# Performance work log

Measured on AMD Instinct MI355X. Metric: run time of the kernel, lower is better.

## Reference

```python
import jax, jax.numpy as jnp
import numpy as np

N_NODES = 50000
N_EDGES = 800000
D_IN = 128
D_OUT = 128


def setup_inputs() -> dict:
    key = jax.random.key(0)
    k1, k2, k3, k4, k5, k6 = jax.random.split(key, 6)
    curr_fea = jax.random.normal(k1, (N_NODES, D_IN), dtype=jnp.float32)
    edge_index = jax.random.randint(k2, (2, N_EDGES), 0, N_NODES, dtype=jnp.int64)
    s = 1.0 / np.sqrt(D_IN)
    W_self = jax.random.uniform(k3, (D_OUT, D_IN), jnp.float32, -s, s)
    b_self = jax.random.uniform(k4, (D_OUT,), jnp.float32, -s, s)
    W_neig = jax.random.uniform(k5, (D_OUT, D_IN), jnp.float32, -s, s)
    b_neig = jax.random.uniform(k6, (D_OUT,), jnp.float32, -s, s)
    return {"curr_fea": curr_fea, "edge_index": edge_index,
            "W_self": W_self, "b_self": b_self,
            "W_neig": W_neig, "b_neig": b_neig}


def reference(curr_fea, edge_index, W_self, b_self, W_neig, b_neig):
    num_nodes = curr_fea.shape[0]
    src, dst = edge_index[0], edge_index[1]
    # symmetrize: messages flow both directions
    src_all = jnp.concatenate([src, dst], axis=0)  # [2E]
    dst_all = jnp.concatenate([dst, src], axis=0)  # [2E]
    # gather neighbor features then scatter-add into destination nodes
    nei_sum = jax.ops.segment_sum(curr_fea[src_all], dst_all,
                                  num_segments=num_nodes)  # [N, d]
    out = (curr_fea @ W_self.T + b_self) + (nei_sum @ W_neig.T + b_neig)
    return out
```

## Files before the change

### kernel.cpp

```cpp
#include <hip/hip_runtime.h>

#define DD 128
#define BM 64
#define BK 32
#define BKN 64
#define NBMAX 1024
#define ECH 4096
#define CAP 2304

typedef __attribute__((ext_vector_type(8))) short bf16x8;
typedef __attribute__((ext_vector_type(4))) float f32x4;

__device__ __forceinline__ unsigned short f2b(float x) {
    unsigned u = __float_as_uint(x);
    u += 0x7fffu + ((u >> 16) & 1u);
    return (unsigned short)(u >> 16);
}
__device__ __forceinline__ float b2f_lo(unsigned v) { return __uint_as_float(v << 16); }
__device__ __forceinline__ float b2f_hi(unsigned v) { return __uint_as_float(v & 0xffff0000u); }

__global__ void detect_kernel(const unsigned long long* __restrict__ ei,
                              int n64, int* __restrict__ flag) {
    int i = threadIdx.x;
    bool big = (i < n64) && (ei[i] >= (1ULL << 32));
    unsigned long long b = __ballot(big);
    if (i == 0) *flag = (b == 0ULL) ? 1 : 0;
}

__global__ void cvt_fea_kernel(const float* __restrict__ in,
                               unsigned short* __restrict__ out, int n4) {
    int i = blockIdx.x * 256 + threadIdx.x;
    if (i >= n4) return;
    float4 v = reinterpret_cast<const float4*>(in)[i];
    ushort4 o;
    o.x = f2b(v.x); o.y = f2b(v.y); o.z = f2b(v.z); o.w = f2b(v.w);
    reinterpret_cast<ushort4*>(out)[i] = o;
}

__global__ void cvt_w_kernel(const float* __restrict__ Ws,
                             const float* __restrict__ Wn,
                             unsigned short* __restrict__ Wcat) {
    int i = blockIdx.x * 256 + threadIdx.x;
    int n = i >> 8, k = i & 255;
    float v = (k < DD) ? Ws[n * DD + k] : Wn[n * DD + (k - DD)];
    Wcat[i] = f2b(v);
}

__launch_bounds__(256)
__global__ void bin_kernel(const void* __restrict__ ei_raw, int E,
                           const int* __restrict__ flag,
                           unsigned* __restrict__ region,
                           unsigned* __restrict__ gcur, int nbk) {
    __shared__ unsigned stage[2 * ECH];
    __shared__ unsigned cnt[NBMAX];
    __shared__ unsigned start[NBMAX];
    __shared__ unsigned cursor[NBMAX];
    __shared__ unsigned gbase[NBMAX];
    __shared__ unsigned scanT[256];

    const int t = threadIdx.x;
    for (int b = t; b < NBMAX; b += 256) { cnt[b] = 0; cursor[b] = 0; gbase[b] = 0; }
    __syncthreads();

    const int e0 = blockIdx.x * ECH;
    const int rf = *flag;
    int es[16], ed[16];
#pragma unroll
    for (int j = 0; j < 16; ++j) {
        int e = e0 + j * 256 + t;
        if (e < E) {
            if (rf) {
                const long long* p = (const long long*)ei_raw;
                es[j] = (int)p[e]; ed[j] = (int)p[e + E];
            } else {
                const int* p = (const int*)ei_raw;
                es[j] = p[e]; ed[j] = p[e + E];
            }
            atomicAdd(&cnt[ed[j] >> 6], 1u);
            atomicAdd(&cnt[es[j] >> 6], 1u);
        } else {
            es[j] = -1; ed[j] = -1;
        }
    }
    __syncthreads();

    unsigned lv[4]; unsigned lsum = 0;
#pragma unroll
    for (int j = 0; j < 4; ++j) { lv[j] = cnt[t * 4 + j]; lsum += lv[j]; }
    scanT[t] = lsum; __syncthreads();
    for (int o = 1; o < 256; o <<= 1) {
        unsigned x = (t >= o) ? scanT[t - o] : 0;
        __syncthreads();
        scanT[t] += x;
        __syncthreads();
    }
    unsigned run = scanT[t] - lsum;
#pragma unroll
    for (int j = 0; j < 4; ++j) { start[t * 4 + j] = run; run += lv[j]; }
    __syncthreads();

#pragma unroll
    for (int j = 0; j < 16; ++j) {
        if (es[j] >= 0) {
            int s = es[j], d = ed[j];
            unsigned p0 = atomicAdd(&cursor[d >> 6], 1u);
            stage[start[d >> 6] + p0] = (unsigned)(d & 63) | ((unsigned)s << 6);
            unsigned p1 = atomicAdd(&cursor[s >> 6], 1u);
            stage[start[s >> 6] + p1] = (unsigned)(s & 63) | ((unsigned)d << 6);
        }
    }
    __syncthreads();

    for (int b = t; b < nbk; b += 256) {
        unsigned c = cnt[b];
        if (c) gbase[b] = atomicAdd(&gcur[b], c);
    }
    __syncthreads();

    const int w = t >> 6, lane = t & 63;
    for (int b = w; b < nbk; b += 4) {
        unsigned c = cnt[b];
        if (!c) continue;
        unsigned gb = gbase[b], st = start[b];
        for (unsigned l2 = lane; l2 < c; l2 += 64) {
            unsigned idx = gb + l2;
            if (idx < CAP)
                region[(size_t)b * CAP + idx] = stage[st + l2];
        }
    }
}

__launch_bounds__(256)
__global__ void nodesort_kernel(unsigned* __restrict__ region,
                                const unsigned* __restrict__ gcur,
                                unsigned* __restrict__ off32, int M) {
    __shared__ unsigned ent[CAP];
    __shared__ unsigned srt[CAP];
    __shared__ unsigned c64[BKN];
    __shared__ unsigned p64[BKN + 1];
    __shared__ unsigned cur64[BKN];

    const int t = threadIdx.x, b = blockIdx.x;
    unsigned cnt = gcur[b];
    if (cnt > CAP) cnt = CAP;
    unsigned* reg = region + (size_t)b * CAP;

    for (unsigned i = t; i < cnt; i += 256) ent[i] = reg[i];
    if (t < BKN) { c64[t] = 0; cur64[t] = 0; }
    __syncthreads();

    for (unsigned i = t; i < cnt; i += 256) atomicAdd(&c64[ent[i] & 63u], 1u);
    __syncthreads();

    if (t == 0) {
        unsigned r = 0;
        for (int n = 0; n < BKN; ++n) { p64[n] = r; r += c64[n]; }
        p64[BKN] = r;
    }
    __syncthreads();

    if (t < BKN) {
        int g = b * BKN + t;
        if (g < M) off32[g] = p64[t] | (c64[t] << 12);
    }

    for (unsigned i = t; i < cnt; i += 256) {
        unsigned e = ent[i];
        unsigned p = atomicAdd(&cur64[e & 63u], 1u);
        srt[p64[e & 63u] + p] = e >> 6;
    }
    __syncthreads();

    for (unsigned i = t; i < cnt; i += 256) reg[i] = srt[i];
}

__launch_bounds__(256)
__global__ void gather_r_kernel(const unsigned short* __restrict__ feaB,
                                const unsigned* __restrict__ region,
                                const unsigned* __restrict__ off32,
                                unsigned short* __restrict__ neiB, int N) {
    int w = (int)((blockIdx.x * 256 + threadIdx.x) >> 6);
    if (w >= N) return;
    int lane = threadIdx.x & 63;
    unsigned v = off32[w];
    const unsigned* lp = region + (size_t)(w >> 6) * CAP + (v & 4095u);
    unsigned cnt = v >> 12;
    float ax = 0.f, ay = 0.f;
    const unsigned short* base = feaB + lane * 2;
    unsigned j = 0;
    for (; j + 8 <= cnt; j += 8) {
        unsigned s0 = lp[j], s1 = lp[j+1], s2 = lp[j+2], s3 = lp[j+3];
        unsigned s4 = lp[j+4], s5 = lp[j+5], s6 = lp[j+6], s7 = lp[j+7];
        unsigned a0 = *reinterpret_cast<const unsigned*>(base + (size_t)s0 * DD);
        unsigned a1 = *reinterpret_cast<const unsigned*>(base + (size_t)s1 * DD);
        unsigned a2 = *reinterpret_cast<const unsigned*>(base + (size_t)s2 * DD);
        unsigned a3 = *reinterpret_cast<const unsigned*>(base + (size_t)s3 * DD);
        unsigned a4 = *reinterpret_cast<const unsigned*>(base + (size_t)s4 * DD);
        unsigned a5 = *reinterpret_cast<const unsigned*>(base + (size_t)s5 * DD);
        unsigned a6 = *reinterpret_cast<const unsigned*>(base + (size_t)s6 * DD);
        unsigned a7 = *reinterpret_cast<const unsigned*>(base + (size_t)s7 * DD);
        ax += b2f_lo(a0) + b2f_lo(a1) + b2f_lo(a2) + b2f_lo(a3)
            + b2f_lo(a4) + b2f_lo(a5) + b2f_lo(a6) + b2f_lo(a7);
        ay += b2f_hi(a0) + b2f_hi(a1) + b2f_hi(a2) + b2f_hi(a3)
            + b2f_hi(a4) + b2f_hi(a5) + b2f_hi(a6) + b2f_hi(a7);
    }
    for (; j < cnt; ++j) {
        unsigned a = *reinterpret_cast<const unsigned*>(base + (size_t)lp[j] * DD);
        ax += b2f_lo(a); ay += b2f_hi(a);
    }
    ushort2 o; o.x = f2b(ax); o.y = f2b(ay);
    *reinterpret_cast<ushort2*>(neiB + (size_t)w * DD + lane * 2) = o;
}

__global__ void transpose_kernel(const float* __restrict__ Ws,
                                 const float* __restrict__ Wn,
                                 float* __restrict__ Wts,
                                 float* __restrict__ Wtn) {
    int idx = blockIdx.x * blockDim.x + threadIdx.x;
    int i = idx & (DD * DD - 1);
    int col = i >> 7;
    int k = i & (DD - 1);
    if (idx < DD * DD)          Wts[k * DD + col] = Ws[i];
    else if (idx < 2 * DD * DD) Wtn[k * DD + col] = Wn[i];
}

__global__ void hist_kernel(const void* __restrict__ ei_raw,
                            int* __restrict__ deg, int E,
                            const int* __restrict__ flag) {
    int e = blockIdx.x * 256 + threadIdx.x;
    if (e >= E) return;
    int s, d;
    if (*flag) {
        const long long* ei = (const long long*)ei_raw;
        s = (int)ei[e]; d = (int)ei[e + E];
    } else {
        const int* ei = (const int*)ei_raw;
        s = ei[e]; d = ei[e + E];
    }
    atomicAdd(&deg[s], 1);
    atomicAdd(&deg[d], 1);
}

__global__ void scan1_kernel(const int* __restrict__ deg, int* __restrict__ off,
                             int* __restrict__ bsum, int N) {
    __shared__ int sd[256];
    int base = blockIdx.x * 1024;
    int t = threadIdx.x;
    int v[4]; int s = 0;
#pragma unroll
    for (int j = 0; j < 4; ++j) {
        int idx = base + t * 4 + j;
        v[j] = (idx < N) ? deg[idx] : 0;
        s += v[j];
    }
    sd[t] = s; __syncthreads();
    for (int o = 1; o < 256; o <<= 1) {
        int x = (t >= o) ? sd[t - o] : 0;
        __syncthreads();
        sd[t] += x;
        __syncthreads();
    }
    int run = sd[t] - s;
    if (t == 255) bsum[blockIdx.x] = sd[255];
#pragma unroll
    for (int j = 0; j < 4; ++j) {
        int idx = base + t * 4 + j;
        if (idx < N) off[idx] = run;
        run += v[j];
    }
}

__global__ void scan2_kernel(int* __restrict__ bsum, int NB,
                             int* __restrict__ total) {
    __shared__ int sd[256];
    int t = threadIdx.x;
    int v = (t < NB) ? bsum[t] : 0;
    sd[t] = v; __syncthreads();
    for (int o = 1; o < 256; o <<= 1) {
        int x = (t >= o) ? sd[t - o] : 0;
        __syncthreads();
        sd[t] += x;
        __syncthreads();
    }
    if (t < NB) bsum[t] = sd[t] - v;
    if (t == 255) *total = sd[255];
}

__global__ void scan3_kernel(int* __restrict__ off, const int* __restrict__ bsum,
                             int N) {
    int i = blockIdx.x * blockDim.x + threadIdx.x;
    if (i < N) off[i] += bsum[i >> 10];
}

__global__ void fill_kernel(const void* __restrict__ ei_raw,
                            const int* __restrict__ off,
                            int* __restrict__ cursor, int* __restrict__ list,
                            int E, const int* __restrict__ flag) {
    int e = blockIdx.x * 256 + threadIdx.x;
    if (e >= E) return;
    int s, d;
    if (*flag) {
        const long long* ei = (const long long*)ei_raw;
        s = (int)ei[e]; d = (int)ei[e + E];
    } else {
        const int* ei = (const int*)ei_raw;
        s = ei[e]; d = ei[e + E];
    }
    int p0 = atomicAdd(&cursor[d], 1); list[off[d] + p0] = s;
    int p1 = atomicAdd(&cursor[s], 1); list[off[s] + p1] = d;
}

__launch_bounds__(256)
__global__ void gather_b_kernel(const unsigned short* __restrict__ feaB,
                                const int* __restrict__ off,
                                const int* __restrict__ list,
                                unsigned short* __restrict__ neiB, int N) {
    int w = (int)((blockIdx.x * 256 + threadIdx.x) >> 6);
    if (w >= N) return;
    int lane = threadIdx.x & 63;
    int start = off[w], end = off[w + 1];
    float ax = 0.f, ay = 0.f;
    const unsigned short* base = feaB + lane * 2;
    int j = start;
    for (; j + 4 <= end; j += 4) {
        int s0 = list[j], s1 = list[j + 1], s2 = list[j + 2], s3 = list[j + 3];
        unsigned a = *reinterpret_cast<const unsigned*>(base + (size_t)s0 * DD);
        unsigned b = *reinterpret_cast<const unsigned*>(base + (size_t)s1 * DD);
        unsigned c = *reinterpret_cast<const unsigned*>(base + (size_t)s2 * DD);
        unsigned d = *reinterpret_cast<const unsigned*>(base + (size_t)s3 * DD);
        ax += b2f_lo(a) + b2f_lo(b) + b2f_lo(c) + b2f_lo(d);
        ay += b2f_hi(a) + b2f_hi(b) + b2f_hi(c) + b2f_hi(d);
    }
    for (; j < end; ++j) {
        unsigned a = *reinterpret_cast<const unsigned*>(base + (size_t)list[j] * DD);
        ax += b2f_lo(a); ay += b2f_hi(a);
    }
    ushort2 o; o.x = f2b(ax); o.y = f2b(ay);
    *reinterpret_cast<ushort2*>(neiB + (size_t)w * DD + lane * 2) = o;
}

__launch_bounds__(256)
__global__ void gather_f32_kernel(const float* __restrict__ fea,
                                  const int* __restrict__ off,
                                  const int* __restrict__ list,
                                  float* __restrict__ nei, int N) {
    int w = (int)((blockIdx.x * 256 + threadIdx.x) >> 6);
    if (w >= N) return;
    int lane = threadIdx.x & 63;
    int start = off[w], end = off[w + 1];
    float2 acc = make_float2(0.f, 0.f);
    const float* base = fea + (size_t)lane * 2;
    int j = start;
    for (; j + 4 <= end; j += 4) {
        int s0 = list[j], s1 = list[j + 1], s2 = list[j + 2], s3 = list[j + 3];
        float2 a = *reinterpret_cast<const float2*>(base + (size_t)s0 * DD);
        float2 b = *reinterpret_cast<const float2*>(base + (size_t)s1 * DD);
        float2 c = *reinterpret_cast<const float2*>(base + (size_t)s2 * DD);
        float2 e = *reinterpret_cast<const float2*>(base + (size_t)s3 * DD);
        acc.x += a.x + b.x + c.x + e.x;
        acc.y += a.y + b.y + c.y + e.y;
    }
    for (; j < end; ++j) {
        float2 a = *reinterpret_cast<const float2*>(base + (size_t)list[j] * DD);
        acc.x += a.x; acc.y += a.y;
    }
    *reinterpret_cast<float2*>(nei + (size_t)w * DD + lane * 2) = acc;
}

__global__ void scatter_kernel(const float* __restrict__ fea,
                               const void* __restrict__ ei_raw,
                               float* __restrict__ nei,
                               int E, const int* __restrict__ flag) {
    long long r = (long long)blockIdx.x * 8 + (threadIdx.x >> 5);
    if (r >= 2LL * E) return;
    int lr = threadIdx.x & 31;
    int i = (int)(r < E ? r : r - E);
    int s, d;
    if (*flag) {
        const long long* ei = (const long long*)ei_raw;
        s = (int)ei[i]; d = (int)ei[i + E];
    } else {
        const int* ei = (const int*)ei_raw;
        s = ei[i]; d = ei[i + E];
    }
    if (r >= E) { int t = s; s = d; d = t; }
    const float4 v = *reinterpret_cast<const float4*>(fea + (size_t)s * DD + lr * 4);
    float* p = nei + (size_t)d * DD + lr * 4;
    unsafeAtomicAdd(p + 0, v.x);
    unsafeAtomicAdd(p + 1, v.y);
    unsafeAtomicAdd(p + 2, v.z);
    unsafeAtomicAdd(p + 3, v.w);
}

__launch_bounds__(256)
__global__ void gemm_mfma_kernel(const unsigned short* __restrict__ feaB,
                                 const unsigned short* __restrict__ neiB,
                                 const unsigned short* __restrict__ Wcat,
                                 const float* __restrict__ bs,
                                 const float* __restrict__ bn,
                                 float* __restrict__ out, int M) {
    const int w  = threadIdx.x >> 6;
    const int l  = threadIdx.x & 63;
    const int lr = l & 15;
    const int ks = l >> 4;
    const int row0 = blockIdx.x * 128 + w * 32;
    const int col0 = blockIdx.y * 64;

    f32x4 acc[2][4] = {};

#pragma unroll
    for (int kb = 0; kb < 256; kb += 32) {
        const unsigned short* A = (kb < DD) ? feaB : neiB;
        const int klocal = (kb < DD) ? kb : kb - DD;
        bf16x8 a[2];
#pragma unroll
        for (int ri = 0; ri < 2; ++ri) {
            int rowg = row0 + ri * 16 + lr;
            if (rowg < M)
                a[ri] = *reinterpret_cast<const bf16x8*>(
                    A + (size_t)rowg * DD + klocal + ks * 8);
            else
                a[ri] = bf16x8{0, 0, 0, 0, 0, 0, 0, 0};
        }
#pragma unroll
        for (int ci = 0; ci < 4; ++ci) {
            int n = col0 + ci * 16 + lr;
            bf16x8 b = *reinterpret_cast<const bf16x8*>(
                Wcat + (size_t)n * 256 + kb + ks * 8);
#pragma unroll
            for (int ri = 0; ri < 2; ++ri)
                acc[ri][ci] = __builtin_amdgcn_mfma_f32_16x16x32_bf16(
                    a[ri], b, acc[ri][ci], 0, 0, 0);
        }
    }

#pragma unroll
    for (int ci = 0; ci < 4; ++ci) {
        int colg = col0 + ci * 16 + lr;
        float bias = bs[colg] + bn[colg];
#pragma unroll
        for (int ri = 0; ri < 2; ++ri) {
            int rbase = row0 + ri * 16 + ks * 4;
#pragma unroll
            for (int i = 0; i < 4; ++i) {
                int rowg = rbase + i;
                if (rowg < M)
                    out[(size_t)rowg * DD + colg] = acc[ri][ci][i] + bias;
            }
        }
    }
}

__launch_bounds__(256)
__global__ void gemm_kernel(const float* __restrict__ fea,
                            const float* __restrict__ nei,
                            const float* __restrict__ Wts,
                            const float* __restrict__ Wtn,
                            const float* __restrict__ bs,
                            const float* __restrict__ bn,
                            float* __restrict__ out, int M) {
    __shared__ float Fs[BM][BK + 4];
    __shared__ float Ns[BM][BK + 4];
    __shared__ float WsT[BK][DD];
    __shared__ float WnT[BK][DD];

    const int t = threadIdx.x;
    const int cg = t & 31;
    const int rg = t >> 5;
    const int row0 = blockIdx.x * BM;

    float4 acc[8];
#pragma unroll
    for (int r = 0; r < 8; ++r) acc[r] = make_float4(0.f, 0.f, 0.f, 0.f);

    for (int kb = 0; kb < DD; kb += BK) {
#pragma unroll
        for (int j = 0; j < 2; ++j) {
            int idx = t + j * 256;
            int row = idx >> 3;
            int seg = idx & 7;
            int grow = row0 + row;
            float4 fv = make_float4(0.f, 0.f, 0.f, 0.f);
            float4 nv = make_float4(0.f, 0.f, 0.f, 0.f);
            if (grow < M) {
                fv = *reinterpret_cast<const float4*>(fea + (size_t)grow * DD + kb + seg * 4);
                nv = *reinterpret_cast<const float4*>(nei + (size_t)grow * DD + kb + seg * 4);
            }
            *reinterpret_cast<float4*>(&Fs[row][seg * 4]) = fv;
            *reinterpret_cast<float4*>(&Ns[row][seg * 4]) = nv;
        }
#pragma unroll
        for (int j = 0; j < 4; ++j) {
            int idx = t + j * 256;
            int kk = idx >> 5;
            int seg = idx & 31;
            *reinterpret_cast<float4*>(&WsT[kk][seg * 4]) =
                *reinterpret_cast<const float4*>(Wts + (size_t)(kb + kk) * DD + seg * 4);
            *reinterpret_cast<float4*>(&WnT[kk][seg * 4]) =
                *reinterpret_cast<const float4*>(Wtn + (size_t)(kb + kk) * DD + seg * 4);
        }
        __syncthreads();

#pragma unroll
        for (int kk = 0; kk < BK; ++kk) {
            float4 wsv = *reinterpret_cast<const float4*>(&WsT[kk][cg * 4]);
            float4 wnv = *reinterpret_cast<const float4*>(&WnT[kk][cg * 4]);
#pragma unroll
            for (int r = 0; r < 8; ++r) {
                float a = Fs[rg * 8 + r][kk];
                float b = Ns[rg * 8 + r][kk];
                acc[r].x += a * wsv.x + b * wnv.x;
                acc[r].y += a * wsv.y + b * wnv.y;
                acc[r].z += a * wsv.z + b * wnv.z;
                acc[r].w += a * wsv.w + b * wnv.w;
            }
        }
        __syncthreads();
    }

    float4 bsv = *reinterpret_cast<const float4*>(bs + cg * 4);
    float4 bnv = *reinterpret_cast<const float4*>(bn + cg * 4);
    float4 bias = make_float4(bsv.x + bnv.x, bsv.y + bnv.y, bsv.z + bnv.z, bsv.w + bnv.w);
#pragma unroll
    for (int r = 0; r < 8; ++r) {
        int grow = row0 + rg * 8 + r;
        if (grow < M) {
            float4 o = make_float4(acc[r].x + bias.x, acc[r].y + bias.y,
                                   acc[r].z + bias.z, acc[r].w + bias.w);
            *reinterpret_cast<float4*>(out + (size_t)grow * DD + cg * 4) = o;
        }
    }
}

extern "C" void kernel_launch(void* const* d_in, const int* in_sizes, int n_in,
                              void* d_out, int out_size, void* d_ws, size_t ws_size,
                              hipStream_t stream) {
    const float* fea = (const float*)d_in[0];
    const void*  ei  = d_in[1];
    const float* Ws  = (const float*)d_in[2];
    const float* bsv = (const float*)d_in[3];
    const float* Wn  = (const float*)d_in[4];
    const float* bnv = (const float*)d_in[5];

    const int M = in_sizes[0] / DD;
    const int E = in_sizes[1] / 2;
    float* out = (float*)d_out;
    char* ws = (char*)d_ws;
    int* flag = (int*)ws;

    const int NBK = (M + BKN - 1) / BKN;
    const size_t csr_bytes = (size_t)M * 8 + (size_t)(M + 1) * 4 + 4096
                           + (size_t)2 * E * 4;

    size_t o1 = 256;
    unsigned short* Wcat = (unsigned short*)(ws + o1); o1 += (size_t)DD * 256 * 2;
    unsigned short* feaB = (unsigned short*)(ws + o1); o1 += (size_t)M * DD * 2;
    unsigned short* neiB = (unsigned short*)(ws + o1); o1 += (size_t)M * DD * 2;
    unsigned* gcur  = (unsigned*)(ws + o1);            o1 += 4096;
    unsigned* region = (unsigned*)(ws + o1);           o1 += (size_t)NBK * CAP * 4;
    unsigned* off32 = (unsigned*)(ws + o1);            o1 += (size_t)NBK * BKN * 4;
    size_t need1 = o1;

    size_t o2 = 256 + (size_t)DD * 256 * 2 + (size_t)2 * M * DD * 2;
    size_t need2 = o2 + csr_bytes;

    size_t o3 = 256;
    float* Wts = (float*)(ws + o3); o3 += (size_t)DD * DD * 4;
    float* Wtn = (float*)(ws + o3); o3 += (size_t)DD * DD * 4;
    size_t need3 = o3 + csr_bytes;

    detect_kernel<<<1, 64, 0, stream>>>((const unsigned long long*)ei,
                                        E < 64 ? E : 64, flag);

    const int NB = (M + 1023) / 1024;
    const int eb = (E + 255) / 256;
    const int n4 = M * DD / 4;

    if (ws_size >= need1 && NBK <= NBMAX) {
        cvt_fea_kernel<<<(n4 + 255) / 256, 256, 0, stream>>>(fea, feaB, n4);
        cvt_w_kernel<<<(DD * 256 + 255) / 256, 256, 0, stream>>>(Ws, Wn, Wcat);
        hipMemsetAsync(gcur, 0, 4096, stream);
        int abks = (E + ECH - 1) / ECH;
        bin_kernel<<<abks, 256, 0, stream>>>(ei, E, flag, region, gcur, NBK);
        nodesort_kernel<<<NBK, 256, 0, stream>>>(region, gcur, off32, M);
        gather_r_kernel<<<(M + 3) / 4, 256, 0, stream>>>(feaB, region, off32, neiB, M);
        dim3 g((M + 127) / 128, 2);
        gemm_mfma_kernel<<<g, 256, 0, stream>>>(feaB, neiB, Wcat, bsv, bnv, out, M);
    } else if (ws_size >= need2) {
        int* deg    = (int*)(ws + o2);
        int* cursor = deg + M;
        int* off    = cursor + M;
        int* bsum   = off + (M + 1);
        int* list   = bsum + 1024;

        cvt_fea_kernel<<<(n4 + 255) / 256, 256, 0, stream>>>(fea, feaB, n4);
        cvt_w_kernel<<<(DD * 256 + 255) / 256, 256, 0, stream>>>(Ws, Wn, Wcat);
        hipMemsetAsync(deg, 0, (size_t)2 * M * 4, stream);
        hist_kernel<<<eb, 256, 0, stream>>>(ei, deg, E, flag);
        scan1_kernel<<<NB, 256, 0, stream>>>(deg, off, bsum, M);
        scan2_kernel<<<1, 256, 0, stream>>>(bsum, NB, &off[M]);
        scan3_kernel<<<(M + 255) / 256, 256, 0, stream>>>(off, bsum, M);
        fill_kernel<<<eb, 256, 0, stream>>>(ei, off, cursor, list, E, flag);
        gather_b_kernel<<<(M + 3) / 4, 256, 0, stream>>>(feaB, off, list, neiB, M);
        dim3 g((M + 127) / 128, 2);
        gemm_mfma_kernel<<<g, 256, 0, stream>>>(feaB, neiB, Wcat, bsv, bnv, out, M);
    } else if (ws_size >= need3) {
        int* deg    = (int*)(ws + o3);
        int* cursor = deg + M;
        int* off    = cursor + M;
        int* bsum   = off + (M + 1);
        int* list   = bsum + 1024;
        float* nei = out;

        transpose_kernel<<<(2 * DD * DD + 255) / 256, 256, 0, stream>>>(Ws, Wn, Wts, Wtn);
        hipMemsetAsync(deg, 0, (size_t)2 * M * 4, stream);
        hist_kernel<<<eb, 256, 0, stream>>>(ei, deg, E, flag);
        scan1_kernel<<<NB, 256, 0, stream>>>(deg, off, bsum, M);
        scan2_kernel<<<1, 256, 0, stream>>>(bsum, NB, &off[M]);
        scan3_kernel<<<(M + 255) / 256, 256, 0, stream>>>(off, bsum, M);
        fill_kernel<<<eb, 256, 0, stream>>>(ei, off, cursor, list, E, flag);
        gather_f32_kernel<<<(M + 3) / 4, 256, 0, stream>>>(fea, off, list, nei, M);
        gemm_kernel<<<(M + BM - 1) / BM, 256, 0, stream>>>(fea, nei, Wts, Wtn,
                                                           bsv, bnv, out, M);
    } else {
        float* nei = out;
        transpose_kernel<<<(2 * DD * DD + 255) / 256, 256, 0, stream>>>(Ws, Wn, Wts, Wtn);
        hipMemsetAsync(nei, 0, (size_t)M * DD * 4, stream);
        long long rows = 2LL * E;
        int sblocks = (int)((rows + 7) / 8);
        scatter_kernel<<<sblocks, 256, 0, stream>>>(fea, ei, nei, E, flag);
        gemm_kernel<<<(M + BM - 1) / BM, 256, 0, stream>>>(fea, nei, Wts, Wtn,
                                                           bsv, bnv, out, M);
    }
}
```

Baseline: 230.7 us.

## Fuse node sort with neighbor gather and merge conversion and detect kernels

The per-bucket node sort and the neighbor gather become one kernel: sorted source lists stay in shared memory, so the write-back of the region and the off32 table are no longer needed. The gather now has two half-waves each loading ushort4 rows and combining them with a shuffle. Feature and weight conversion are merged into one launch, and the int64 detection is folded into bin_kernel, which now runs with 512 threads and smaller edge chunks. Fewer launches and less global traffic are the aim. The risks are that only one block per bucket now does all the gather work for 64 nodes, which lowers parallelism, and that every bin block re-reads the 64 detection words.

```diff
diff --git a/kernel.cpp b/kernel.cpp
--- a/kernel.cpp
+++ b/kernel.cpp
@@ -5,7 +5,7 @@
 #define BK 32
 #define BKN 64
 #define NBMAX 1024
-#define ECH 4096
+#define ECH 2048
 #define CAP 2304
 
 typedef __attribute__((ext_vector_type(8))) short bf16x8;
@@ -18,6 +18,16 @@
 }
 __device__ __forceinline__ float b2f_lo(unsigned v) { return __uint_as_float(v << 16); }
 __device__ __forceinline__ float b2f_hi(unsigned v) { return __uint_as_float(v & 0xffff0000u); }
+__device__ __forceinline__ float bf(unsigned short u) {
+    return __uint_as_float((unsigned)u << 16);
+}
+
+__device__ __forceinline__ int detect_rf(const void* ei_raw, int E, int lane) {
+    const unsigned long long* p = (const unsigned long long*)ei_raw;
+    int n64 = E < 64 ? E : 64;
+    bool big = (lane < n64) && (p[lane] >= (1ULL << 32));
+    return (__ballot(big) == 0ULL) ? 1 : 0;
+}
 
 __global__ void detect_kernel(const unsigned long long* __restrict__ ei,
                               int n64, int* __restrict__ flag) {
@@ -25,6 +35,29 @@
     bool big = (i < n64) && (ei[i] >= (1ULL << 32));
     unsigned long long b = __ballot(big);
     if (i == 0) *flag = (b == 0ULL) ? 1 : 0;
+}
+
+__global__ void cvt_all_kernel(const float* __restrict__ fea,
+                               const float* __restrict__ Ws,
+                               const float* __restrict__ Wn,
+                               unsigned short* __restrict__ feaB,
+                               unsigned short* __restrict__ Wcat, int n4) {
+    int i = blockIdx.x * 256 + threadIdx.x;
+    if (i < n4) {
+        float4 v = reinterpret_cast<const float4*>(fea)[i];
+        ushort4 o;
+        o.x = f2b(v.x); o.y = f2b(v.y); o.z = f2b(v.z); o.w = f2b(v.w);
+        reinterpret_cast<ushort4*>(feaB)[i] = o;
+    } else if (i < n4 + 2 * DD * DD / 4) {
+        int k4 = i - n4;
+        int n = k4 >> 6;
+        int kk = (k4 & 63) * 4;
+        float4 v = (kk < DD) ? *reinterpret_cast<const float4*>(Ws + n * DD + kk)
+                             : *reinterpret_cast<const float4*>(Wn + n * DD + kk - DD);
+        ushort4 o;
+        o.x = f2b(v.x); o.y = f2b(v.y); o.z = f2b(v.z); o.w = f2b(v.w);
+        reinterpret_cast<ushort4*>(Wcat)[k4] = o;
+    }
 }
 
 __global__ void cvt_fea_kernel(const float* __restrict__ in,
@@ -46,9 +79,8 @@
     Wcat[i] = f2b(v);
 }
 
-__launch_bounds__(256)
+__launch_bounds__(512)
 __global__ void bin_kernel(const void* __restrict__ ei_raw, int E,
-                           const int* __restrict__ flag,
                            unsigned* __restrict__ region,
                            unsigned* __restrict__ gcur, int nbk) {
     __shared__ unsigned stage[2 * ECH];
@@ -56,18 +88,20 @@
     __shared__ unsigned start[NBMAX];
     __shared__ unsigned cursor[NBMAX];
     __shared__ unsigned gbase[NBMAX];
-    __shared__ unsigned scanT[256];
+    __shared__ unsigned scanT[512];
 
     const int t = threadIdx.x;
-    for (int b = t; b < NBMAX; b += 256) { cnt[b] = 0; cursor[b] = 0; gbase[b] = 0; }
+    const int lane = t & 63;
+    const int rf = detect_rf(ei_raw, E, lane);
+
+    for (int b = t; b < NBMAX; b += 512) { cnt[b] = 0; cursor[b] = 0; }
     __syncthreads();
 
     const int e0 = blockIdx.x * ECH;
-    const int rf = *flag;
-    int es[16], ed[16];
-#pragma unroll
-    for (int j = 0; j < 16; ++j) {
-        int e = e0 + j * 256 + t;
+    int es[4], ed[4];
+#pragma unroll
+    for (int j = 0; j < 4; ++j) {
+        int e = e0 + j * 512 + t;
         if (e < E) {
             if (rf) {
                 const long long* p = (const long long*)ei_raw;
@@ -84,11 +118,11 @@
     }
     __syncthreads();
 
-    unsigned lv[4]; unsigned lsum = 0;
-#pragma unroll
-    for (int j = 0; j < 4; ++j) { lv[j] = cnt[t * 4 + j]; lsum += lv[j]; }
+    unsigned lv[2]; unsigned lsum = 0;
+#pragma unroll
+    for (int j = 0; j < 2; ++j) { lv[j] = cnt[t * 2 + j]; lsum += lv[j]; }
     scanT[t] = lsum; __syncthreads();
-    for (int o = 1; o < 256; o <<= 1) {
+    for (int o = 1; o < 512; o <<= 1) {
         unsigned x = (t >= o) ? scanT[t - o] : 0;
         __syncthreads();
         scanT[t] += x;
@@ -96,11 +130,11 @@
     }
     unsigned run = scanT[t] - lsum;
 #pragma unroll
-    for (int j = 0; j < 4; ++j) { start[t * 4 + j] = run; run += lv[j]; }
-    __syncthreads();
-
-#pragma unroll
-    for (int j = 0; j < 16; ++j) {
+    for (int j = 0; j < 2; ++j) { start[t * 2 + j] = run; run += lv[j]; }
+    __syncthreads();
+
+#pragma unroll
+    for (int j = 0; j < 4; ++j) {
         if (es[j] >= 0) {
             int s = es[j], d = ed[j];
             unsigned p0 = atomicAdd(&cursor[d >> 6], 1u);
@@ -111,14 +145,14 @@
     }
     __syncthreads();
 
-    for (int b = t; b < nbk; b += 256) {
+    for (int b = t; b < nbk; b += 512) {
         unsigned c = cnt[b];
-        if (c) gbase[b] = atomicAdd(&gcur[b], c);
-    }
-    __syncthreads();
-
-    const int w = t >> 6, lane = t & 63;
-    for (int b = w; b < nbk; b += 4) {
+        gbase[b] = c ? atomicAdd(&gcur[b], c) : 0;
+    }
+    __syncthreads();
+
+    const int w = t >> 6;
+    for (int b = w; b < nbk; b += 8) {
         unsigned c = cnt[b];
         if (!c) continue;
         unsigned gb = gbase[b], st = start[b];
@@ -130,10 +164,11 @@
     }
 }
 
-__launch_bounds__(256)
-__global__ void nodesort_kernel(unsigned* __restrict__ region,
-                                const unsigned* __restrict__ gcur,
-                                unsigned* __restrict__ off32, int M) {
+__launch_bounds__(512)
+__global__ void gather_sort_kernel(const unsigned short* __restrict__ feaB,
+                                   const unsigned* __restrict__ region,
+                                   const unsigned* __restrict__ gcur,
+                                   unsigned short* __restrict__ neiB, int M) {
     __shared__ unsigned ent[CAP];
     __shared__ unsigned srt[CAP];
     __shared__ unsigned c64[BKN];
@@ -143,13 +178,13 @@
     const int t = threadIdx.x, b = blockIdx.x;
     unsigned cnt = gcur[b];
     if (cnt > CAP) cnt = CAP;
-    unsigned* reg = region + (size_t)b * CAP;
-
-    for (unsigned i = t; i < cnt; i += 256) ent[i] = reg[i];
+    const unsigned* reg = region + (size_t)b * CAP;
+
+    for (unsigned i = t; i < cnt; i += 512) ent[i] = reg[i];
     if (t < BKN) { c64[t] = 0; cur64[t] = 0; }
     __syncthreads();
 
-    for (unsigned i = t; i < cnt; i += 256) atomicAdd(&c64[ent[i] & 63u], 1u);
+    for (unsigned i = t; i < cnt; i += 512) atomicAdd(&c64[ent[i] & 63u], 1u);
     __syncthreads();
 
     if (t == 0) {
@@ -159,57 +194,57 @@
     }
     __syncthreads();
 
-    if (t < BKN) {
-        int g = b * BKN + t;
-        if (g < M) off32[g] = p64[t] | (c64[t] << 12);
-    }
-
-    for (unsigned i = t; i < cnt; i += 256) {
+    for (unsigned i = t; i < cnt; i += 512) {
         unsigned e = ent[i];
         unsigned p = atomicAdd(&cur64[e & 63u], 1u);
         srt[p64[e & 63u] + p] = e >> 6;
     }
     __syncthreads();
 
-    for (unsigned i = t; i < cnt; i += 256) reg[i] = srt[i];
-}
-
-__launch_bounds__(256)
-__global__ void gather_r_kernel(const unsigned short* __restrict__ feaB,
-                                const unsigned* __restrict__ region,
-                                const unsigned* __restrict__ off32,
-                                unsigned short* __restrict__ neiB, int N) {
-    int w = (int)((blockIdx.x * 256 + threadIdx.x) >> 6);
-    if (w >= N) return;
-    int lane = threadIdx.x & 63;
-    unsigned v = off32[w];
-    const unsigned* lp = region + (size_t)(w >> 6) * CAP + (v & 4095u);
-    unsigned cnt = v >> 12;
-    float ax = 0.f, ay = 0.f;
-    const unsigned short* base = feaB + lane * 2;
-    unsigned j = 0;
-    for (; j + 8 <= cnt; j += 8) {
-        unsigned s0 = lp[j], s1 = lp[j+1], s2 = lp[j+2], s3 = lp[j+3];
-        unsigned s4 = lp[j+4], s5 = lp[j+5], s6 = lp[j+6], s7 = lp[j+7];
-        unsigned a0 = *reinterpret_cast<const unsigned*>(base + (size_t)s0 * DD);
-        unsigned a1 = *reinterpret_cast<const unsigned*>(base + (size_t)s1 * DD);
-        unsigned a2 = *reinterpret_cast<const unsigned*>(base + (size_t)s2 * DD);
-        unsigned a3 = *reinterpret_cast<const unsigned*>(base + (size_t)s3 * DD);
-        unsigned a4 = *reinterpret_cast<const unsigned*>(base + (size_t)s4 * DD);
-        unsigned a5 = *reinterpret_cast<const unsigned*>(base + (size_t)s5 * DD);
-        unsigned a6 = *reinterpret_cast<const unsigned*>(base + (size_t)s6 * DD);
-        unsigned a7 = *reinterpret_cast<const unsigned*>(base + (size_t)s7 * DD);
-        ax += b2f_lo(a0) + b2f_lo(a1) + b2f_lo(a2) + b2f_lo(a3)
-            + b2f_lo(a4) + b2f_lo(a5) + b2f_lo(a6) + b2f_lo(a7);
-        ay += b2f_hi(a0) + b2f_hi(a1) + b2f_hi(a2) + b2f_hi(a3)
-            + b2f_hi(a4) + b2f_hi(a5) + b2f_hi(a6) + b2f_hi(a7);
-    }
-    for (; j < cnt; ++j) {
-        unsigned a = *reinterpret_cast<const unsigned*>(base + (size_t)lp[j] * DD);
-        ax += b2f_lo(a); ay += b2f_hi(a);
-    }
-    ushort2 o; o.x = f2b(ax); o.y = f2b(ay);
-    *reinterpret_cast<ushort2*>(neiB + (size_t)w * DD + lane * 2) = o;
+    const int w = t >> 6, lane = t & 63;
+    const int half = lane >> 5, li = lane & 31;
+    const unsigned short* bp = feaB + li * 4;
+
+    for (int n = w; n < BKN; n += 8) {
+        int g = b * BKN + n;
+        if (g >= M) break;
+        unsigned p = p64[n], d = c64[n];
+        float a0 = 0.f, a1 = 0.f, a2 = 0.f, a3 = 0.f;
+        unsigned j = 0;
+        for (; j + 8 <= d; j += 8) {
+            unsigned s0 = srt[p + j + half];
+            unsigned s1 = srt[p + j + 2 + half];
+            unsigned s2 = srt[p + j + 4 + half];
+            unsigned s3 = srt[p + j + 6 + half];
+            ushort4 v0 = *reinterpret_cast<const ushort4*>(bp + (size_t)s0 * DD);
+            ushort4 v1 = *reinterpret_cast<const ushort4*>(bp + (size_t)s1 * DD);
+            ushort4 v2 = *reinterpret_cast<const ushort4*>(bp + (size_t)s2 * DD);
+            ushort4 v3 = *reinterpret_cast<const ushort4*>(bp + (size_t)s3 * DD);
+            a0 += bf(v0.x) + bf(v1.x) + bf(v2.x) + bf(v3.x);
+            a1 += bf(v0.y) + bf(v1.y) + bf(v2.y) + bf(v3.y);
+            a2 += bf(v0.z) + bf(v1.z) + bf(v2.z) + bf(v3.z);
+            a3 += bf(v0.w) + bf(v1.w) + bf(v2.w) + bf(v3.w);
+        }
+        for (; j + 2 <= d; j += 2) {
+            unsigned s = srt[p + j + half];
+            ushort4 v = *reinterpret_cast<const ushort4*>(bp + (size_t)s * DD);
+            a0 += bf(v.x); a1 += bf(v.y); a2 += bf(v.z); a3 += bf(v.w);
+        }
+        if (j < d && half == 0) {
+            unsigned s = srt[p + j];
+            ushort4 v = *reinterpret_cast<const ushort4*>(bp + (size_t)s * DD);
+            a0 += bf(v.x); a1 += bf(v.y); a2 += bf(v.z); a3 += bf(v.w);
+        }
+        a0 += __shfl_xor(a0, 32);
+        a1 += __shfl_xor(a1, 32);
+        a2 += __shfl_xor(a2, 32);
+        a3 += __shfl_xor(a3, 32);
+        if (half == 0) {
+            ushort4 o;
+            o.x = f2b(a0); o.y = f2b(a1); o.z = f2b(a2); o.w = f2b(a3);
+            *reinterpret_cast<ushort4*>(neiB + (size_t)g * DD + li * 4) = o;
+        }
+    }
 }
 
 __global__ void transpose_kernel(const float* __restrict__ Ws,
@@ -558,7 +593,6 @@
     unsigned short* neiB = (unsigned short*)(ws + o1); o1 += (size_t)M * DD * 2;
     unsigned* gcur  = (unsigned*)(ws + o1);            o1 += 4096;
     unsigned* region = (unsigned*)(ws + o1);           o1 += (size_t)NBK * CAP * 4;
-    unsigned* off32 = (unsigned*)(ws + o1);            o1 += (size_t)NBK * BKN * 4;
     size_t need1 = o1;
 
     size_t o2 = 256 + (size_t)DD * 256 * 2 + (size_t)2 * M * DD * 2;
@@ -569,21 +603,17 @@
     float* Wtn = (float*)(ws + o3); o3 += (size_t)DD * DD * 4;
     size_t need3 = o3 + csr_bytes;
 
-    detect_kernel<<<1, 64, 0, stream>>>((const unsigned long long*)ei,
-                                        E < 64 ? E : 64, flag);
-
     const int NB = (M + 1023) / 1024;
     const int eb = (E + 255) / 256;
     const int n4 = M * DD / 4;
 
     if (ws_size >= need1 && NBK <= NBMAX) {
-        cvt_fea_kernel<<<(n4 + 255) / 256, 256, 0, stream>>>(fea, feaB, n4);
-        cvt_w_kernel<<<(DD * 256 + 255) / 256, 256, 0, stream>>>(Ws, Wn, Wcat);
         hipMemsetAsync(gcur, 0, 4096, stream);
+        int cvtb = (n4 + 2 * DD * DD / 4 + 255) / 256;
+        cvt_all_kernel<<<cvtb, 256, 0, stream>>>(fea, Ws, Wn, feaB, Wcat, n4);
         int abks = (E + ECH - 1) / ECH;
-        bin_kernel<<<abks, 256, 0, stream>>>(ei, E, flag, region, gcur, NBK);
-        nodesort_kernel<<<NBK, 256, 0, stream>>>(region, gcur, off32, M);
-        gather_r_kernel<<<(M + 3) / 4, 256, 0, stream>>>(feaB, region, off32, neiB, M);
+        bin_kernel<<<abks, 512, 0, stream>>>(ei, E, region, gcur, NBK);
+        gather_sort_kernel<<<NBK, 512, 0, stream>>>(feaB, region, gcur, neiB, M);
         dim3 g((M + 127) / 128, 2);
         gemm_mfma_kernel<<<g, 256, 0, stream>>>(feaB, neiB, Wcat, bsv, bnv, out, M);
     } else if (ws_size >= need2) {
@@ -593,6 +623,8 @@
         int* bsum   = off + (M + 1);
         int* list   = bsum + 1024;
 
+        detect_kernel<<<1, 64, 0, stream>>>((const unsigned long long*)ei,
+                                            E < 64 ? E : 64, flag);
         cvt_fea_kernel<<<(n4 + 255) / 256, 256, 0, stream>>>(fea, feaB, n4);
         cvt_w_kernel<<<(DD * 256 + 255) / 256, 256, 0, stream>>>(Ws, Wn, Wcat);
         hipMemsetAsync(deg, 0, (size_t)2 * M * 4, stream);
@@ -612,6 +644,8 @@
         int* list   = bsum + 1024;
         float* nei = out;
 
+        detect_kernel<<<1, 64, 0, stream>>>((const unsigned long long*)ei,
+                                            E < 64 ? E : 64, flag);
         transpose_kernel<<<(2 * DD * DD + 255) / 256, 256, 0, stream>>>(Ws, Wn, Wts, Wtn);
         hipMemsetAsync(deg, 0, (size_t)2 * M * 4, stream);
         hist_kernel<<<eb, 256, 0, stream>>>(ei, deg, E, flag);
@@ -624,6 +658,8 @@
                                                            bsv, bnv, out, M);
     } else {
         float* nei = out;
+        detect_kernel<<<1, 64, 0, stream>>>((const unsigned long long*)ei,
+                                            E < 64 ? E : 64, flag);
         transpose_kernel<<<(2 * DD * DD + 255) / 256, 256, 0, stream>>>(Ws, Wn, Wts, Wtn);
         hipMemsetAsync(nei, 0, (size_t)M * DD * 4, stream);
         long long rows = 2LL * E;
```

New measurement: 205.6 us. 1.12x faster.
